# Kernel tuning notes

Measured on AMD Instinct MI355X. Metric: run time of the kernel, lower is better.

Reference implementation:

```python
import jax, jax.numpy as jnp
import numpy as np

T, B, S, F, V = 128, 512, 512, 8, 100  # tgt_size, batch, src_seq, n_fields, mr vocab


def setup_inputs() -> dict:
    key = jax.random.key(0)
    k0, k1, k2, k3 = jax.random.split(key, 4)
    attention = jax.random.uniform(k0, (T, B, S), dtype=jnp.float32)
    gates = jax.random.uniform(k1, (F, B, T), dtype=jnp.float32)  # teacher gates per field
    mrs = jax.random.randint(k2, (B, S), 0, V)
    field_map = jax.random.randint(k3, (V,), 0, F + 1)  # 0 = unmapped, 1..F = field index
    return {"attention": attention, "gates": gates, "mrs": mrs, "field_map": field_map}


def reference(attention, gates, mrs, field_map):
    # field index per (batch, src_step); 0 means 'no field' -> zero column
    fidx = field_map[mrs]                              # [B, S]
    # prepend a zero 'field' so index 0 gathers zeros
    g = jnp.concatenate(
        [jnp.zeros((1,) + gates.shape[1:], gates.dtype), gates], axis=0
    )                                                  # [F+1, B, T]
    b_idx = jnp.arange(gates.shape[1])[:, None]        # [B, 1]
    unnorm = g[fidx, b_idx]                            # [B, S, T]
    unnorm = jnp.transpose(unnorm, (2, 0, 1))          # [T, B, S]
    normalizer = unnorm.sum(axis=2, keepdims=True)     # [T, B, 1]
    normalizer = jnp.where(normalizer == 0, jnp.ones_like(normalizer), normalizer)
    reference_attention = unnorm / normalizer
    return jnp.mean((reference_attention - attention) ** 2)
```

## Files before the change

kernel.cpp:

```cpp
#include <hip/hip_runtime.h>

#define T_DIM 128
#define B_DIM 512
#define S_DIM 512
#define F_DIM 8
#define TCHUNK 16

__global__ __launch_bounds__(256) void hist_kernel(const int* __restrict__ mrs,
                                                   const int* __restrict__ field_map,
                                                   float* __restrict__ counts,
                                                   float* __restrict__ out) {
    __shared__ int h[F_DIM + 1];
    const int b = blockIdx.x;
    const int tid = threadIdx.x;
    if (tid <= F_DIM) h[tid] = 0;
    if (b == 0 && tid == 0) out[0] = 0.0f;
    __syncthreads();
    const int base = b * S_DIM + tid * 2;
    const int f0 = field_map[mrs[base]];
    const int f1 = field_map[mrs[base + 1]];
    atomicAdd(&h[f0], 1);
    atomicAdd(&h[f1], 1);
    __syncthreads();
    if (tid < F_DIM) counts[b * F_DIM + tid] = (float)h[tid + 1];
}

__global__ __launch_bounds__(256) void lut_kernel(const float* __restrict__ gates,
                                                  const float* __restrict__ counts,
                                                  float* __restrict__ glut) {
    const int idx = blockIdx.x * blockDim.x + threadIdx.x;
    const int t = idx & (T_DIM - 1);
    const int b = idx >> 7;
    float g[F_DIM];
    float norm = 0.0f;
#pragma unroll
    for (int f = 0; f < F_DIM; ++f) {
        g[f] = gates[((size_t)f * B_DIM + b) * T_DIM + t];
        norm = fmaf(counts[b * F_DIM + f], g[f], norm);
    }
    const float inv = (norm == 0.0f) ? 1.0f : (1.0f / norm);
    float* o = glut + (size_t)idx * 9;
    o[0] = 0.0f;
#pragma unroll
    for (int f = 0; f < F_DIM; ++f) o[f + 1] = g[f] * inv;
}

__global__ __launch_bounds__(256) void loss_kernel(const float* __restrict__ attn,
                                                   const int* __restrict__ mrs,
                                                   const int* __restrict__ field_map,
                                                   const float* __restrict__ glut,
                                                   float* __restrict__ out) {
    const int b = blockIdx.x;
    const int tc = blockIdx.y;
    const int tid = threadIdx.x;
    const int s0 = tid * 2;

    const int mbase = b * S_DIM + s0;
    const int f0 = field_map[mrs[mbase]];
    const int f1 = field_map[mrs[mbase + 1]];

    float acc = 0.0f;
    const int t0 = tc * TCHUNK;
    const float* arow = attn + ((size_t)t0 * B_DIM + b) * S_DIM + s0;
    const float* lrow = glut + ((size_t)b * T_DIM + t0) * 9;
#pragma unroll
    for (int i = 0; i < TCHUNK; ++i) {
        const float2 v = *(const float2*)arow;
        const float g0 = lrow[f0];
        const float g1 = lrow[f1];
        const float d0 = v.x - g0;
        const float d1 = v.y - g1;
        acc = fmaf(d0, d0, acc);
        acc = fmaf(d1, d1, acc);
        arow += (size_t)B_DIM * S_DIM;
        lrow += 9;
    }

#pragma unroll
    for (int off = 32; off > 0; off >>= 1) acc += __shfl_down(acc, off);
    __shared__ float wsum[4];
    if ((tid & 63) == 0) wsum[tid >> 6] = acc;
    __syncthreads();
    if (tid == 0) {
        const float s = (wsum[0] + wsum[1]) + (wsum[2] + wsum[3]);
        atomicAdd(out, s * (1.0f / ((float)T_DIM * (float)B_DIM * (float)S_DIM)));
    }
}

extern "C" void kernel_launch(void* const* d_in, const int* in_sizes, int n_in,
                              void* d_out, int out_size, void* d_ws, size_t ws_size,
                              hipStream_t stream) {
    const float* attention = (const float*)d_in[0];
    const float* gates     = (const float*)d_in[1];
    const int*   mrs       = (const int*)d_in[2];
    const int*   field_map = (const int*)d_in[3];
    float* out = (float*)d_out;

    float* counts = (float*)d_ws;
    float* glut   = (float*)((char*)d_ws + 16384);

    hist_kernel<<<dim3(B_DIM), dim3(256), 0, stream>>>(mrs, field_map, counts, out);
    lut_kernel<<<dim3((B_DIM * T_DIM) / 256), dim3(256), 0, stream>>>(gates, counts, glut);
    loss_kernel<<<dim3(B_DIM, T_DIM / TCHUNK), dim3(256), 0, stream>>>(attention, mrs, field_map,
                                                                       glut, out);
}
```

Before: 211.9 us.

## Fuse histogram, LUT and loss kernels into one kernel with shared-memory LUT

Measured after the change: 210.2 us. Within noise of the previous version (-0.8%).

```diff
diff --git a/kernel.cpp b/kernel.cpp
--- a/kernel.cpp
+++ b/kernel.cpp
@@ -6,79 +6,75 @@
 #define F_DIM 8
 #define TCHUNK 16
 
-__global__ __launch_bounds__(256) void hist_kernel(const int* __restrict__ mrs,
-                                                   const int* __restrict__ field_map,
-                                                   float* __restrict__ counts,
-                                                   float* __restrict__ out) {
+__global__ void zero_kernel(float* __restrict__ out) { out[0] = 0.0f; }
+
+__global__ __launch_bounds__(256) void fused_kernel(const float* __restrict__ attn,
+                                                    const float* __restrict__ gates,
+                                                    const int* __restrict__ mrs,
+                                                    const int* __restrict__ field_map,
+                                                    float* __restrict__ out) {
+    const int b = blockIdx.x;
+    const int t0 = blockIdx.y * TCHUNK;
+    const int tid = threadIdx.x;
+    const int lo = tid & 127;
+    const int hi = tid >> 7;
+
     __shared__ int h[F_DIM + 1];
-    const int b = blockIdx.x;
-    const int tid = threadIdx.x;
+    __shared__ float glds[F_DIM][TCHUNK];
+    __shared__ float lut[TCHUNK][F_DIM + 1];
+    __shared__ float wsum[4];
+
     if (tid <= F_DIM) h[tid] = 0;
-    if (b == 0 && tid == 0) out[0] = 0.0f;
     __syncthreads();
-    const int base = b * S_DIM + tid * 2;
-    const int f0 = field_map[mrs[base]];
-    const int f1 = field_map[mrs[base + 1]];
-    atomicAdd(&h[f0], 1);
-    atomicAdd(&h[f1], 1);
+
+    const int4 m = *(const int4*)(mrs + b * S_DIM + lo * 4);
+    const int f0 = field_map[m.x];
+    const int f1 = field_map[m.y];
+    const int f2 = field_map[m.z];
+    const int f3 = field_map[m.w];
+    if (hi == 0) {
+        atomicAdd(&h[f0], 1);
+        atomicAdd(&h[f1], 1);
+        atomicAdd(&h[f2], 1);
+        atomicAdd(&h[f3], 1);
+    }
+
+    if (tid < F_DIM * TCHUNK) {
+        const int f = tid >> 4;
+        const int i = tid & 15;
+        glds[f][i] = gates[((size_t)f * B_DIM + b) * T_DIM + t0 + i];
+    }
     __syncthreads();
-    if (tid < F_DIM) counts[b * F_DIM + tid] = (float)h[tid + 1];
-}
 
-__global__ __launch_bounds__(256) void lut_kernel(const float* __restrict__ gates,
-                                                  const float* __restrict__ counts,
-                                                  float* __restrict__ glut) {
-    const int idx = blockIdx.x * blockDim.x + threadIdx.x;
-    const int t = idx & (T_DIM - 1);
-    const int b = idx >> 7;
-    float g[F_DIM];
-    float norm = 0.0f;
+    if (tid < TCHUNK) {
+        float norm = 0.0f;
 #pragma unroll
-    for (int f = 0; f < F_DIM; ++f) {
-        g[f] = gates[((size_t)f * B_DIM + b) * T_DIM + t];
-        norm = fmaf(counts[b * F_DIM + f], g[f], norm);
+        for (int f = 0; f < F_DIM; ++f) norm = fmaf((float)h[f + 1], glds[f][tid], norm);
+        const float inv = (norm == 0.0f) ? 1.0f : 1.0f / norm;
+        lut[tid][0] = 0.0f;
+#pragma unroll
+        for (int f = 0; f < F_DIM; ++f) lut[tid][f + 1] = glds[f][tid] * inv;
     }
-    const float inv = (norm == 0.0f) ? 1.0f : (1.0f / norm);
-    float* o = glut + (size_t)idx * 9;
-    o[0] = 0.0f;
-#pragma unroll
-    for (int f = 0; f < F_DIM; ++f) o[f + 1] = g[f] * inv;
-}
-
-__global__ __launch_bounds__(256) void loss_kernel(const float* __restrict__ attn,
-                                                   const int* __restrict__ mrs,
-                                                   const int* __restrict__ field_map,
-                                                   const float* __restrict__ glut,
-                                                   float* __restrict__ out) {
-    const int b = blockIdx.x;
-    const int tc = blockIdx.y;
-    const int tid = threadIdx.x;
-    const int s0 = tid * 2;
-
-    const int mbase = b * S_DIM + s0;
-    const int f0 = field_map[mrs[mbase]];
-    const int f1 = field_map[mrs[mbase + 1]];
+    __syncthreads();
 
     float acc = 0.0f;
-    const int t0 = tc * TCHUNK;
-    const float* arow = attn + ((size_t)t0 * B_DIM + b) * S_DIM + s0;
-    const float* lrow = glut + ((size_t)b * T_DIM + t0) * 9;
 #pragma unroll
-    for (int i = 0; i < TCHUNK; ++i) {
-        const float2 v = *(const float2*)arow;
-        const float g0 = lrow[f0];
-        const float g1 = lrow[f1];
-        const float d0 = v.x - g0;
-        const float d1 = v.y - g1;
+    for (int i = 0; i < TCHUNK / 2; ++i) {
+        const int t = t0 + 2 * i + hi;
+        const float4 v = *(const float4*)(attn + ((size_t)t * B_DIM + b) * S_DIM + lo * 4);
+        const float* L = lut[2 * i + hi];
+        const float d0 = v.x - L[f0];
+        const float d1 = v.y - L[f1];
+        const float d2 = v.z - L[f2];
+        const float d3 = v.w - L[f3];
         acc = fmaf(d0, d0, acc);
         acc = fmaf(d1, d1, acc);
-        arow += (size_t)B_DIM * S_DIM;
-        lrow += 9;
+        acc = fmaf(d2, d2, acc);
+        acc = fmaf(d3, d3, acc);
     }
 
 #pragma unroll
     for (int off = 32; off > 0; off >>= 1) acc += __shfl_down(acc, off);
-    __shared__ float wsum[4];
     if ((tid & 63) == 0) wsum[tid >> 6] = acc;
     __syncthreads();
     if (tid == 0) {
@@ -96,11 +92,7 @@
     const int*   field_map = (const int*)d_in[3];
     float* out = (float*)d_out;
 
-    float* counts = (float*)d_ws;
-    float* glut   = (float*)((char*)d_ws + 16384);
-
-    hist_kernel<<<dim3(B_DIM), dim3(256), 0, stream>>>(mrs, field_map, counts, out);
-    lut_kernel<<<dim3((B_DIM * T_DIM) / 256), dim3(256), 0, stream>>>(gates, counts, glut);
-    loss_kernel<<<dim3(B_DIM, T_DIM / TCHUNK), dim3(256), 0, stream>>>(attention, mrs, field_map,
-                                                                       glut, out);
+    zero_kernel<<<dim3(1), dim3(1), 0, stream>>>(out);
+    fused_kernel<<<dim3(B_DIM, T_DIM / TCHUNK), dim3(256), 0, stream>>>(attention, gates, mrs,
+                                                                        field_map, out);
 }
```
